# Optimization experiments

Hardware: AMD Instinct MI355X
Metric: run time of the kernel (lower is better)

## Reference

```python
import jax, jax.numpy as jnp
import numpy as np

B, S, H, E, V = 128, 400, 256, 128, 50000
PAD = 250  # extended-vocab padding hard-coded in the torch module


def setup_inputs() -> dict:
    key = jax.random.key(0)
    ks = jax.random.split(key, 20)
    return {
        "input_token": jax.random.randint(ks[0], (B, 1), 0, V),
        "last_decoder_hidden": jax.random.normal(ks[1], (B, H), jnp.float32),
        "encoder_states": jax.random.normal(ks[2], (B, S, H), jnp.float32),
        "full_input_var": jax.random.randint(ks[3], (B, S), 0, V + PAD),
        "emb_table": jax.random.normal(ks[4], (V, E), jnp.float32) * 0.02,
        "gru_w_ih": jax.random.normal(ks[5], (3 * H, E), jnp.float32) * 0.05,
        "gru_w_hh": jax.random.normal(ks[6], (3 * H, H), jnp.float32) * 0.05,
        "gru_b_ih": jax.random.normal(ks[7], (3 * H,), jnp.float32) * 0.05,
        "gru_b_hh": jax.random.normal(ks[8], (3 * H,), jnp.float32) * 0.05,
        "w_h": jax.random.normal(ks[9], (H,), jnp.float32),
        "w_s": jax.random.normal(ks[10], (H,), jnp.float32),
        "att_bias": jax.random.normal(ks[11], (1,), jnp.float32),
        "attn_v": jax.random.normal(ks[12], (H,), jnp.float32),
        "gen_w": jax.random.normal(ks[13], (1, 2 * H + E), jnp.float32) * 0.05,
        "gen_b": jax.random.normal(ks[14], (1,), jnp.float32) * 0.05,
        "outh_w": jax.random.normal(ks[15], (E, 2 * H), jnp.float32) * 0.05,
        "outh_b": jax.random.normal(ks[16], (E,), jnp.float32) * 0.05,
        "outv_w": jax.random.normal(ks[17], (V, E), jnp.float32) * 0.05,
        "outv_b": jax.random.normal(ks[18], (V,), jnp.float32) * 0.05,
    }


def reference(input_token, last_decoder_hidden, encoder_states, full_input_var,
              emb_table, gru_w_ih, gru_w_hh, gru_b_ih, gru_b_hh,
              w_h, w_s, att_bias, attn_v, gen_w, gen_b,
              outh_w, outh_b, outv_w, outv_b):
    b, s, h = encoder_states.shape
    v = outv_w.shape[0]
    # Embedding lookup (dropout is identity in eval mode): [B, E]
    x = emb_table[input_token[:, 0]]
    # Single-step GRU cell (PyTorch gate order: r, z, n)
    gi = x @ gru_w_ih.T + gru_b_ih
    gh = last_decoder_hidden @ gru_w_hh.T + gru_b_hh
    i_r, i_z, i_n = jnp.split(gi, 3, axis=-1)
    h_r, h_z, h_n = jnp.split(gh, 3, axis=-1)
    r = jax.nn.sigmoid(i_r + h_r)
    z = jax.nn.sigmoid(i_z + h_z)
    n = jnp.tanh(i_n + r * h_n)
    h_new = (1.0 - z) * n + z * last_decoder_hidden  # [B, H]
    # Bahdanau-style elementwise attention
    att = jnp.tanh(w_h * encoder_states + w_s * h_new[:, None, :] + att_bias)  # [B,S,H]
    scores = jnp.einsum('bsh,h->bs', att, attn_v)
    att_dist = jax.nn.softmax(scores, axis=-1)  # [B, S]
    context = jnp.einsum('bs,bsh->bh', att_dist, encoder_states)  # [B, H]
    dec_ctx = jnp.concatenate([h_new, context], axis=-1)  # [B, 2H]
    p_vocab = jax.nn.softmax((dec_ctx @ outh_w.T + outh_b) @ outv_w.T + outv_b, axis=-1)  # [B, V]
    p_gen = jax.nn.sigmoid(jnp.concatenate([dec_ctx, x], axis=1) @ gen_w.T + gen_b)  # [B, 1]
    # Pointer scatter-add into extended vocab [B, V+PAD]
    rows = jnp.arange(b)[:, None]
    token_input_dist = jnp.zeros((b, v + PAD), p_vocab.dtype).at[rows, full_input_var].add(att_dist)
    p_final = jnp.concatenate([p_vocab * p_gen, jnp.zeros((b, PAD), p_vocab.dtype)], axis=1) \
              + (1.0 - p_gen) * token_input_dist
    return (h_new, p_final, p_gen, p_vocab, att_dist)
```

## Files before the change

### kernel.cpp

```cpp
#include <hip/hip_runtime.h>
#include <hip/hip_bf16.h>


#define B_ 128
#define S_ 400
#define H_ 256
#define E_ 128
#define V_ 50000
#define PAD_ 250
#define VP_ (V_ + PAD_)
#define NC_ 8
#define CS_ (S_ / NC_)
#define NSUM_ 16

typedef unsigned short ushort_t;
typedef __attribute__((ext_vector_type(8))) short bf16x8;
typedef __attribute__((ext_vector_type(4))) float f32x4;

__device__ __forceinline__ unsigned short f2bfu(float f) {
    __hip_bfloat16 h = __float2bfloat16(f);
    union { __hip_bfloat16 h; unsigned short u; } c;
    c.h = h;
    return c.u;
}

__device__ __forceinline__ float sigmoid_fast(float x) {
    return 1.0f / (1.0f + __expf(-x));
}

__device__ __forceinline__ float tanh_fast(float x) {
    return 1.0f - 2.0f / (__expf(2.0f * x) + 1.0f);
}

__device__ __forceinline__ float waveReduceSumAll(float v) {
#pragma unroll
    for (int off = 1; off < 64; off <<= 1) v += __shfl_xor(v, off, 64);
    return v;
}

__global__ __launch_bounds__(256) void k_gates(
    const int* __restrict__ token, const float* __restrict__ emb,
    const float* __restrict__ hprev,
    const float* __restrict__ w_ih, const float* __restrict__ w_hh,
    float* __restrict__ gi_ws, float* __restrict__ gh_ws) {
    __shared__ ushort_t xh[B_ * 264];
    __shared__ int toks[B_];
    int t = threadIdx.x;
    bool isIH = blockIdx.x < 12;
    if (isIH) {
        if (t < B_) toks[t] = token[t];
        __syncthreads();
#pragma unroll
        for (int i = 0; i < 16; i++) {
            int fidx = i * 256 + t;
            int b = fidx >> 5, k4 = fidx & 31;
            float4 q = *(const float4*)(emb + (size_t)toks[b] * E_ + k4 * 4);
            ushort4 u;
            u.x = f2bfu(q.x); u.y = f2bfu(q.y); u.z = f2bfu(q.z); u.w = f2bfu(q.w);
            *(ushort4*)&xh[b * 136 + k4 * 4] = u;
        }
    } else {
#pragma unroll
        for (int i = 0; i < 32; i++) {
            int fidx = i * 256 + t;
            int b = fidx >> 6, k4 = fidx & 63;
            float4 q = *(const float4*)(hprev + (size_t)b * H_ + k4 * 4);
            ushort4 u;
            u.x = f2bfu(q.x); u.y = f2bfu(q.y); u.z = f2bfu(q.z); u.w = f2bfu(q.w);
            *(ushort4*)&xh[b * 264 + k4 * 4] = u;
        }
    }
    __syncthreads();

    int wave = t >> 6, lane = t & 63, lm = lane & 15, quad = lane >> 4;
    int tile = (isIH ? blockIdx.x : blockIdx.x - 12) * 4 + wave;
    int v = tile * 16 + lm;
    int K = isIH ? E_ : H_;
    int pitch = isIH ? 136 : 264;
    const float* wrow = (isIH ? w_ih : w_hh) + (size_t)v * K;
    float* gout = isIH ? gi_ws : gh_ws;

    f32x4 acc[8];
#pragma unroll
    for (int bt = 0; bt < 8; bt++) acc[bt] = (f32x4){0.f, 0.f, 0.f, 0.f};

    for (int kc = 0; kc < (K >> 5); kc++) {
        int k0 = kc * 32 + quad * 8;
        float4 w0 = *(const float4*)(wrow + k0);
        float4 w1 = *(const float4*)(wrow + k0 + 4);
        bf16x8 bf;
        bf[0] = (short)f2bfu(w0.x); bf[1] = (short)f2bfu(w0.y);
        bf[2] = (short)f2bfu(w0.z); bf[3] = (short)f2bfu(w0.w);
        bf[4] = (short)f2bfu(w1.x); bf[5] = (short)f2bfu(w1.y);
        bf[6] = (short)f2bfu(w1.z); bf[7] = (short)f2bfu(w1.w);
#pragma unroll
        for (int bt = 0; bt < 8; bt++) {
            bf16x8 af = *(const bf16x8*)&xh[(bt * 16 + lm) * pitch + k0];
            acc[bt] = __builtin_amdgcn_mfma_f32_16x16x32_bf16(af, bf, acc[bt], 0, 0, 0);
        }
    }
#pragma unroll
    for (int bt = 0; bt < 8; bt++)
#pragma unroll
        for (int r = 0; r < 4; r++) {
            int b = bt * 16 + quad * 4 + r;
            gout[(size_t)b * 768 + v] = acc[bt][r];
        }
}

__global__ __launch_bounds__(256) void k_attn(
    const float* __restrict__ gi_ws, const float* __restrict__ gh_ws,
    const float* __restrict__ b_ih, const float* __restrict__ b_hh,
    const float* __restrict__ hprev,
    const float* __restrict__ enc,
    const float* __restrict__ w_h, const float* __restrict__ w_s,
    const float* __restrict__ att_bias, const float* __restrict__ attn_v,
    float* __restrict__ out_hnew,
    float* __restrict__ sc_ws, float* __restrict__ ml_ws, float* __restrict__ ctxp_ws) {
    int c = blockIdx.x, b = blockIdx.y;
    int t = threadIdx.x;
    int wave = t >> 6, lane = t & 63;
    __shared__ float whs[H_], vs[H_], cs[H_], cmerge[H_];
    __shared__ float mred[4], lred[4];

    {
        float ir = gi_ws[(size_t)b * 768 + t] + b_ih[t];
        float iz = gi_ws[(size_t)b * 768 + 256 + t] + b_ih[256 + t];
        float in_ = gi_ws[(size_t)b * 768 + 512 + t] + b_ih[512 + t];
        float hr = gh_ws[(size_t)b * 768 + t] + b_hh[t];
        float hz = gh_ws[(size_t)b * 768 + 256 + t] + b_hh[256 + t];
        float hn = gh_ws[(size_t)b * 768 + 512 + t] + b_hh[512 + t];
        float hp = hprev[(size_t)b * H_ + t];
        float r = sigmoid_fast(ir + hr);
        float z = sigmoid_fast(iz + hz);
        float n = tanh_fast(in_ + r * hn);
        float h = (1.0f - z) * n + z * hp;
        if (c == 0) out_hnew[(size_t)b * H_ + t] = h;
        whs[t] = w_h[t];
        vs[t] = attn_v[t];
        cs[t] = w_s[t] * h + att_bias[0];
        cmerge[t] = 0.0f;
    }
    __syncthreads();

    int h0 = lane * 4;
    float m_w = -1e30f, l_w = 0.0f;
    float cx0 = 0.f, cx1 = 0.f, cx2 = 0.f, cx3 = 0.f;
    for (int si = wave; si < CS_; si += 4) {
        int s = c * CS_ + si;
        float4 u = *(const float4*)(enc + ((size_t)(b * S_ + s)) * H_ + h0);
        float p = vs[h0 + 0] * tanh_fast(whs[h0 + 0] * u.x + cs[h0 + 0])
                + vs[h0 + 1] * tanh_fast(whs[h0 + 1] * u.y + cs[h0 + 1])
                + vs[h0 + 2] * tanh_fast(whs[h0 + 2] * u.z + cs[h0 + 2])
                + vs[h0 + 3] * tanh_fast(whs[h0 + 3] * u.w + cs[h0 + 3]);
        p = waveReduceSumAll(p);
        if (lane == 0) sc_ws[b * S_ + s] = p;
        float mn = fmaxf(m_w, p);
        float scale = __expf(m_w - mn);
        float w = __expf(p - mn);
        cx0 = cx0 * scale + w * u.x;
        cx1 = cx1 * scale + w * u.y;
        cx2 = cx2 * scale + w * u.z;
        cx3 = cx3 * scale + w * u.w;
        l_w = l_w * scale + w;
        m_w = mn;
    }
    if (lane == 0) mred[wave] = m_w;
    __syncthreads();
    float m_c = fmaxf(fmaxf(mred[0], mred[1]), fmaxf(mred[2], mred[3]));
    float wf = __expf(m_w - m_c);
    if (lane == 0) lred[wave] = l_w * wf;
    atomicAdd(&cmerge[h0 + 0], cx0 * wf);
    atomicAdd(&cmerge[h0 + 1], cx1 * wf);
    atomicAdd(&cmerge[h0 + 2], cx2 * wf);
    atomicAdd(&cmerge[h0 + 3], cx3 * wf);
    __syncthreads();
    if (t == 0) {
        ml_ws[(b * NC_ + c) * 2 + 0] = m_c;
        ml_ws[(b * NC_ + c) * 2 + 1] = lred[0] + lred[1] + lred[2] + lred[3];
    }
    ctxp_ws[(size_t)(b * NC_ + c) * H_ + t] = cmerge[t];
}

__global__ __launch_bounds__(1024) void k_combine(
    const float* __restrict__ sc_ws, const float* __restrict__ ml_ws,
    const float* __restrict__ ctxp_ws,
    const float* __restrict__ out_hnew,
    const int* __restrict__ token, const float* __restrict__ emb,
    const float* __restrict__ outh_w, const float* __restrict__ outh_b,
    const float* __restrict__ gen_w, const float* __restrict__ gen_b,
    float* __restrict__ out_attd, float* __restrict__ out_pgen,
    float* __restrict__ attd_ws, float* __restrict__ hidden_ws,
    float* __restrict__ pgen_ws, float* __restrict__ row_sum16) {
    int b = blockIdx.x;
    int t = threadIdx.x;
    int wave = t >> 6, lane = t & 63;
    __shared__ float ml[NC_ * 2];
    __shared__ float dc[2 * H_ + E_];
    __shared__ float r2[16];

    if (b == 0) {
        for (int i = t; i < NSUM_ * B_; i += 1024) row_sum16[i] = 0.0f;
    }
    if (t < NC_ * 2) ml[t] = ml_ws[b * NC_ * 2 + t];
    __syncthreads();
    float M = -1e30f;
#pragma unroll
    for (int c = 0; c < NC_; c++) M = fmaxf(M, ml[2 * c]);
    float L = 0.0f;
#pragma unroll
    for (int c = 0; c < NC_; c++) L += ml[2 * c + 1] * __expf(ml[2 * c] - M);
    float invL = 1.0f / L;

    if (t < S_) {
        float a = __expf(sc_ws[b * S_ + t] - M) * invL;
        attd_ws[b * S_ + t] = a;
        out_attd[(size_t)b * S_ + t] = a;
    }
    if (t < H_) {
        float acc = 0.0f;
#pragma unroll
        for (int c = 0; c < NC_; c++)
            acc += __expf(ml[2 * c] - M) * ctxp_ws[(size_t)(b * NC_ + c) * H_ + t];
        dc[t] = out_hnew[(size_t)b * H_ + t];
        dc[H_ + t] = acc * invL;
    }
    if (t < E_) dc[2 * H_ + t] = emb[(size_t)token[b] * E_ + t];
    __syncthreads();

    {
        int r = t >> 3, sub = t & 7;
        const float* wrow = outh_w + (size_t)r * (2 * H_);
        float acc = 0.0f;
#pragma unroll
        for (int i = 0; i < 16; i++) {
            int k = i * 32 + sub * 4;
            float4 q = *(const float4*)(wrow + k);
            acc += dc[k] * q.x + dc[k + 1] * q.y + dc[k + 2] * q.z + dc[k + 3] * q.w;
        }
        acc += __shfl_down(acc, 4, 64);
        acc += __shfl_down(acc, 2, 64);
        acc += __shfl_down(acc, 1, 64);
        if (sub == 0) hidden_ws[(size_t)b * E_ + r] = acc + outh_b[r];
    }
    float pp = (t < 2 * H_ + E_) ? dc[t] * gen_w[t] : 0.0f;
    pp = waveReduceSumAll(pp);
    if (lane == 0) r2[wave] = pp;
    __syncthreads();
    if (t == 0) {
        float g = 0.0f;
#pragma unroll
        for (int wv = 0; wv < 16; wv++) g += r2[wv];
        g = sigmoid_fast(g + gen_b[0]);
        pgen_ws[b] = g;
        out_pgen[b] = g;
    }
}

#define VT_TOTAL (V_ / 16)
#define HID_PITCH 136
__global__ __launch_bounds__(256) void k_vocab_mfma(
    const float* __restrict__ outv_w, const float* __restrict__ outv_b,
    const float* __restrict__ hidden_ws,
    float* __restrict__ out_pvocab, float* __restrict__ row_sum16) {
    __shared__ ushort_t hid[B_ * HID_PITCH];
    __shared__ float rsum[B_];
    int t = threadIdx.x;

    const float4* h4 = (const float4*)hidden_ws;
#pragma unroll
    for (int i = 0; i < 16; i++) {
        int fidx = i * 256 + t;
        float4 q = h4[fidx];
        int row = fidx >> 5;
        int col = (fidx & 31) << 2;
        ushort4 u;
        u.x = f2bfu(q.x); u.y = f2bfu(q.y); u.z = f2bfu(q.z); u.w = f2bfu(q.w);
        *(ushort4*)&hid[row * HID_PITCH + col] = u;
    }
    if (t < B_) rsum[t] = 0.0f;
    __syncthreads();

    int wave = t >> 6, lane = t & 63, lm = lane & 15, quad = lane >> 4;
    int vt = blockIdx.x * 4 + wave;

    if (vt < VT_TOTAL) {
        int v = vt * 16 + lm;
        const float* wrow = outv_w + (size_t)v * E_;

        f32x4 acc[8];
#pragma unroll
        for (int bt = 0; bt < 8; bt++) acc[bt] = (f32x4){0.f, 0.f, 0.f, 0.f};

#pragma unroll
        for (int kc = 0; kc < 4; kc++) {
            int k0 = kc * 32 + quad * 8;
            float4 w0 = *(const float4*)(wrow + k0);
            float4 w1 = *(const float4*)(wrow + k0 + 4);
            bf16x8 bf;
            bf[0] = (short)f2bfu(w0.x); bf[1] = (short)f2bfu(w0.y);
            bf[2] = (short)f2bfu(w0.z); bf[3] = (short)f2bfu(w0.w);
            bf[4] = (short)f2bfu(w1.x); bf[5] = (short)f2bfu(w1.y);
            bf[6] = (short)f2bfu(w1.z); bf[7] = (short)f2bfu(w1.w);
#pragma unroll
            for (int bt = 0; bt < 8; bt++) {
                bf16x8 af = *(const bf16x8*)&hid[(bt * 16 + lm) * HID_PITCH + k0];
                acc[bt] = __builtin_amdgcn_mfma_f32_16x16x32_bf16(af, bf, acc[bt], 0, 0, 0);
            }
        }

        float bias = outv_b[v];
#pragma unroll
        for (int bt = 0; bt < 8; bt++) {
#pragma unroll
            for (int r = 0; r < 4; r++) {
                int b = bt * 16 + quad * 4 + r;
                float e = __expf(fminf(acc[bt][r] + bias, 60.0f));
                out_pvocab[(size_t)b * V_ + v] = e;
                float s = e;
                s += __shfl_xor(s, 1);
                s += __shfl_xor(s, 2);
                s += __shfl_xor(s, 4);
                s += __shfl_xor(s, 8);
                if (lm == 0) atomicAdd(&rsum[b], s);
            }
        }
    }
    __syncthreads();
    if (t < B_) atomicAdd(&row_sum16[(blockIdx.x & (NSUM_ - 1)) * B_ + t], rsum[t]);
}

__global__ __launch_bounds__(256) void k_final(
    const float* __restrict__ row_sum16, const float* __restrict__ pgen_ws,
    float* __restrict__ out_pfinal, float* __restrict__ out_pvocab) {
    int b = blockIdx.y;
    int jbase = blockIdx.x * 2048;
    int t = threadIdx.x;
    float rs = 0.0f;
#pragma unroll
    for (int i = 0; i < NSUM_; i++) rs += row_sum16[i * B_ + b];
    float inv = 1.0f / rs;
    float pg = pgen_ws[b];
#pragma unroll
    for (int i = 0; i < 8; i++) {
        int j = jbase + i * 256 + t;
        if (j < VP_) {
            if (j < V_) {
                float p = out_pvocab[(size_t)b * V_ + j] * inv;
                out_pvocab[(size_t)b * V_ + j] = p;
                out_pfinal[(size_t)b * VP_ + j] = p * pg;
            } else {
                out_pfinal[(size_t)b * VP_ + j] = 0.0f;
            }
        }
    }
}

__global__ __launch_bounds__(256) void k_scatter(
    const int* __restrict__ fiv, const float* __restrict__ attd_ws,
    const float* __restrict__ pgen_ws, float* __restrict__ out_pfinal) {
    int b = blockIdx.x;
    int t = threadIdx.x;
    float omg = 1.0f - pgen_ws[b];
    for (int s = t; s < S_; s += 256) {
        int idx = fiv[b * S_ + s];
        float val = omg * attd_ws[b * S_ + s];
        atomicAdd(&out_pfinal[(size_t)b * VP_ + idx], val);
    }
}

extern "C" void kernel_launch(void* const* d_in, const int* in_sizes, int n_in,
                              void* d_out, int out_size, void* d_ws, size_t ws_size,
                              hipStream_t stream) {
    const int* token = (const int*)d_in[0];
    const float* hprev = (const float*)d_in[1];
    const float* enc = (const float*)d_in[2];
    const int* fiv = (const int*)d_in[3];
    const float* emb = (const float*)d_in[4];
    const float* w_ih = (const float*)d_in[5];
    const float* w_hh = (const float*)d_in[6];
    const float* b_ih = (const float*)d_in[7];
    const float* b_hh = (const float*)d_in[8];
    const float* w_h = (const float*)d_in[9];
    const float* w_s = (const float*)d_in[10];
    const float* att_bias = (const float*)d_in[11];
    const float* attn_v = (const float*)d_in[12];
    const float* gen_w = (const float*)d_in[13];
    const float* gen_b = (const float*)d_in[14];
    const float* outh_w = (const float*)d_in[15];
    const float* outh_b = (const float*)d_in[16];
    const float* outv_w = (const float*)d_in[17];
    const float* outv_b = (const float*)d_in[18];

    float* out = (float*)d_out;
    float* out_hnew = out;
    float* out_pfinal = out + (size_t)B_ * H_;
    float* out_pgen = out_pfinal + (size_t)B_ * VP_;
    float* out_pvocab = out_pgen + B_;
    float* out_attd = out_pvocab + (size_t)B_ * V_;

    float* wsf = (float*)d_ws;
    float* gi_ws = wsf;
    float* gh_ws = wsf + 98304;
    float* attd_ws = wsf + 196608;
    float* hidden_ws = wsf + 247808;
    float* pgen_ws = wsf + 264192;
    float* row_sum16 = wsf + 264320;
    float* sc_ws = wsf + 266368;
    float* ml_ws = wsf + 317568;
    float* ctxp_ws = wsf + 319616;

    k_gates<<<24, 256, 0, stream>>>(token, emb, hprev, w_ih, w_hh, gi_ws, gh_ws);
    k_attn<<<dim3(NC_, B_), 256, 0, stream>>>(gi_ws, gh_ws, b_ih, b_hh, hprev,
                                              enc, w_h, w_s, att_bias, attn_v,
                                              out_hnew, sc_ws, ml_ws, ctxp_ws);
    k_combine<<<B_, 1024, 0, stream>>>(sc_ws, ml_ws, ctxp_ws, out_hnew, token, emb,
                                       outh_w, outh_b, gen_w, gen_b,
                                       out_attd, out_pgen,
                                       attd_ws, hidden_ws, pgen_ws, row_sum16);
    k_vocab_mfma<<<782, 256, 0, stream>>>(outv_w, outv_b, hidden_ws, out_pvocab, row_sum16);
    k_final<<<dim3(25, B_), 256, 0, stream>>>(row_sum16, pgen_ws, out_pfinal, out_pvocab);
    k_scatter<<<B_, 256, 0, stream>>>(fiv, attd_ws, pgen_ws, out_pfinal);
}
```

Measured before the change: 227.2 us.

## Fuse attention with combine and final normalization with pointer scatter

Merges the chunked attention kernel and the combine kernel into one per-batch 1024-thread block, so scores stay in shared memory and the partial max/sum/context workspaces and their cross-kernel merge go away. It also merges the vocab normalization kernel with the scatter kernel, using float4 loads, and reads p_gen and att_dist from the output buffers. This removes two launches and the workspace round-trips. In exchange the attention grid drops from 1024 blocks to 128 and the final pass from 3200 blocks to 128, so parallelism over the GPU shrinks.

```diff
diff --git a/kernel.cpp b/kernel.cpp
--- a/kernel.cpp
+++ b/kernel.cpp
@@ -9,8 +9,6 @@
 #define V_ 50000
 #define PAD_ 250
 #define VP_ (V_ + PAD_)
-#define NC_ 8
-#define CS_ (S_ / NC_)
 #define NSUM_ 16
 
 typedef unsigned short ushort_t;
@@ -108,22 +106,31 @@
         }
 }
 
-__global__ __launch_bounds__(256) void k_attn(
+__global__ __launch_bounds__(1024) void k_attn_combine(
     const float* __restrict__ gi_ws, const float* __restrict__ gh_ws,
     const float* __restrict__ b_ih, const float* __restrict__ b_hh,
     const float* __restrict__ hprev,
     const float* __restrict__ enc,
     const float* __restrict__ w_h, const float* __restrict__ w_s,
     const float* __restrict__ att_bias, const float* __restrict__ attn_v,
-    float* __restrict__ out_hnew,
-    float* __restrict__ sc_ws, float* __restrict__ ml_ws, float* __restrict__ ctxp_ws) {
-    int c = blockIdx.x, b = blockIdx.y;
+    const int* __restrict__ token, const float* __restrict__ emb,
+    const float* __restrict__ outh_w, const float* __restrict__ outh_b,
+    const float* __restrict__ gen_w, const float* __restrict__ gen_b,
+    float* __restrict__ out_hnew, float* __restrict__ out_attd,
+    float* __restrict__ out_pgen,
+    float* __restrict__ hidden_ws, float* __restrict__ row_sum16) {
+    int b = blockIdx.x;
     int t = threadIdx.x;
     int wave = t >> 6, lane = t & 63;
     __shared__ float whs[H_], vs[H_], cs[H_], cmerge[H_];
-    __shared__ float mred[4], lred[4];
-
-    {
+    __shared__ float scl[S_];
+    __shared__ float mred[16], lred[16], r2[16];
+    __shared__ float dc[2 * H_ + E_];
+
+    if (b == 0) {
+        for (int i = t; i < NSUM_ * B_; i += 1024) row_sum16[i] = 0.0f;
+    }
+    if (t < H_) {
         float ir = gi_ws[(size_t)b * 768 + t] + b_ih[t];
         float iz = gi_ws[(size_t)b * 768 + 256 + t] + b_ih[256 + t];
         float in_ = gi_ws[(size_t)b * 768 + 512 + t] + b_ih[512 + t];
@@ -135,26 +142,31 @@
         float z = sigmoid_fast(iz + hz);
         float n = tanh_fast(in_ + r * hn);
         float h = (1.0f - z) * n + z * hp;
-        if (c == 0) out_hnew[(size_t)b * H_ + t] = h;
+        out_hnew[(size_t)b * H_ + t] = h;
+        dc[t] = h;
         whs[t] = w_h[t];
         vs[t] = attn_v[t];
         cs[t] = w_s[t] * h + att_bias[0];
         cmerge[t] = 0.0f;
     }
+    if (t < E_) dc[2 * H_ + t] = emb[(size_t)token[b] * E_ + t];
     __syncthreads();
 
     int h0 = lane * 4;
+    float wh0 = whs[h0], wh1 = whs[h0 + 1], wh2 = whs[h0 + 2], wh3 = whs[h0 + 3];
+    float vv0 = vs[h0], vv1 = vs[h0 + 1], vv2 = vs[h0 + 2], vv3 = vs[h0 + 3];
+    float cc0 = cs[h0], cc1 = cs[h0 + 1], cc2 = cs[h0 + 2], cc3 = cs[h0 + 3];
+
     float m_w = -1e30f, l_w = 0.0f;
     float cx0 = 0.f, cx1 = 0.f, cx2 = 0.f, cx3 = 0.f;
-    for (int si = wave; si < CS_; si += 4) {
-        int s = c * CS_ + si;
+    for (int s = wave; s < S_; s += 16) {
         float4 u = *(const float4*)(enc + ((size_t)(b * S_ + s)) * H_ + h0);
-        float p = vs[h0 + 0] * tanh_fast(whs[h0 + 0] * u.x + cs[h0 + 0])
-                + vs[h0 + 1] * tanh_fast(whs[h0 + 1] * u.y + cs[h0 + 1])
-                + vs[h0 + 2] * tanh_fast(whs[h0 + 2] * u.z + cs[h0 + 2])
-                + vs[h0 + 3] * tanh_fast(whs[h0 + 3] * u.w + cs[h0 + 3]);
+        float p = vv0 * tanh_fast(wh0 * u.x + cc0)
+                + vv1 * tanh_fast(wh1 * u.y + cc1)
+                + vv2 * tanh_fast(wh2 * u.z + cc2)
+                + vv3 * tanh_fast(wh3 * u.w + cc3);
         p = waveReduceSumAll(p);
-        if (lane == 0) sc_ws[b * S_ + s] = p;
+        if (lane == 0) scl[s] = p;
         float mn = fmaxf(m_w, p);
         float scale = __expf(m_w - mn);
         float w = __expf(p - mn);
@@ -167,65 +179,25 @@
     }
     if (lane == 0) mred[wave] = m_w;
     __syncthreads();
-    float m_c = fmaxf(fmaxf(mred[0], mred[1]), fmaxf(mred[2], mred[3]));
-    float wf = __expf(m_w - m_c);
+    float M = -1e30f;
+#pragma unroll
+    for (int i = 0; i < 16; i++) M = fmaxf(M, mred[i]);
+    float wf = __expf(m_w - M);
     if (lane == 0) lred[wave] = l_w * wf;
     atomicAdd(&cmerge[h0 + 0], cx0 * wf);
     atomicAdd(&cmerge[h0 + 1], cx1 * wf);
     atomicAdd(&cmerge[h0 + 2], cx2 * wf);
     atomicAdd(&cmerge[h0 + 3], cx3 * wf);
     __syncthreads();
-    if (t == 0) {
-        ml_ws[(b * NC_ + c) * 2 + 0] = m_c;
-        ml_ws[(b * NC_ + c) * 2 + 1] = lred[0] + lred[1] + lred[2] + lred[3];
-    }
-    ctxp_ws[(size_t)(b * NC_ + c) * H_ + t] = cmerge[t];
-}
-
-__global__ __launch_bounds__(1024) void k_combine(
-    const float* __restrict__ sc_ws, const float* __restrict__ ml_ws,
-    const float* __restrict__ ctxp_ws,
-    const float* __restrict__ out_hnew,
-    const int* __restrict__ token, const float* __restrict__ emb,
-    const float* __restrict__ outh_w, const float* __restrict__ outh_b,
-    const float* __restrict__ gen_w, const float* __restrict__ gen_b,
-    float* __restrict__ out_attd, float* __restrict__ out_pgen,
-    float* __restrict__ attd_ws, float* __restrict__ hidden_ws,
-    float* __restrict__ pgen_ws, float* __restrict__ row_sum16) {
-    int b = blockIdx.x;
-    int t = threadIdx.x;
-    int wave = t >> 6, lane = t & 63;
-    __shared__ float ml[NC_ * 2];
-    __shared__ float dc[2 * H_ + E_];
-    __shared__ float r2[16];
-
-    if (b == 0) {
-        for (int i = t; i < NSUM_ * B_; i += 1024) row_sum16[i] = 0.0f;
-    }
-    if (t < NC_ * 2) ml[t] = ml_ws[b * NC_ * 2 + t];
-    __syncthreads();
-    float M = -1e30f;
-#pragma unroll
-    for (int c = 0; c < NC_; c++) M = fmaxf(M, ml[2 * c]);
     float L = 0.0f;
 #pragma unroll
-    for (int c = 0; c < NC_; c++) L += ml[2 * c + 1] * __expf(ml[2 * c] - M);
+    for (int i = 0; i < 16; i++) L += lred[i];
     float invL = 1.0f / L;
 
-    if (t < S_) {
-        float a = __expf(sc_ws[b * S_ + t] - M) * invL;
-        attd_ws[b * S_ + t] = a;
-        out_attd[(size_t)b * S_ + t] = a;
-    }
-    if (t < H_) {
-        float acc = 0.0f;
-#pragma unroll
-        for (int c = 0; c < NC_; c++)
-            acc += __expf(ml[2 * c] - M) * ctxp_ws[(size_t)(b * NC_ + c) * H_ + t];
-        dc[t] = out_hnew[(size_t)b * H_ + t];
-        dc[H_ + t] = acc * invL;
-    }
-    if (t < E_) dc[2 * H_ + t] = emb[(size_t)token[b] * E_ + t];
+    for (int s = t; s < S_; s += 1024) {
+        out_attd[(size_t)b * S_ + s] = __expf(scl[s] - M) * invL;
+    }
+    if (t < H_) dc[H_ + t] = cmerge[t] * invL;
     __syncthreads();
 
     {
@@ -251,9 +223,7 @@
         float g = 0.0f;
 #pragma unroll
         for (int wv = 0; wv < 16; wv++) g += r2[wv];
-        g = sigmoid_fast(g + gen_b[0]);
-        pgen_ws[b] = g;
-        out_pgen[b] = g;
+        out_pgen[b] = sigmoid_fast(g + gen_b[0]);
     }
 }
 
@@ -330,42 +300,35 @@
     if (t < B_) atomicAdd(&row_sum16[(blockIdx.x & (NSUM_ - 1)) * B_ + t], rsum[t]);
 }
 
-__global__ __launch_bounds__(256) void k_final(
-    const float* __restrict__ row_sum16, const float* __restrict__ pgen_ws,
+__global__ __launch_bounds__(1024) void k_final_scatter(
+    const float* __restrict__ row_sum16, const float* __restrict__ pgen,
+    const int* __restrict__ fiv, const float* __restrict__ attd,
     float* __restrict__ out_pfinal, float* __restrict__ out_pvocab) {
-    int b = blockIdx.y;
-    int jbase = blockIdx.x * 2048;
+    int b = blockIdx.x;
     int t = threadIdx.x;
     float rs = 0.0f;
 #pragma unroll
     for (int i = 0; i < NSUM_; i++) rs += row_sum16[i * B_ + b];
     float inv = 1.0f / rs;
-    float pg = pgen_ws[b];
-#pragma unroll
-    for (int i = 0; i < 8; i++) {
-        int j = jbase + i * 256 + t;
-        if (j < VP_) {
-            if (j < V_) {
-                float p = out_pvocab[(size_t)b * V_ + j] * inv;
-                out_pvocab[(size_t)b * V_ + j] = p;
-                out_pfinal[(size_t)b * VP_ + j] = p * pg;
-            } else {
-                out_pfinal[(size_t)b * VP_ + j] = 0.0f;
-            }
-        }
-    }
-}
-
-__global__ __launch_bounds__(256) void k_scatter(
-    const int* __restrict__ fiv, const float* __restrict__ attd_ws,
-    const float* __restrict__ pgen_ws, float* __restrict__ out_pfinal) {
-    int b = blockIdx.x;
-    int t = threadIdx.x;
-    float omg = 1.0f - pgen_ws[b];
-    for (int s = t; s < S_; s += 256) {
-        int idx = fiv[b * S_ + s];
-        float val = omg * attd_ws[b * S_ + s];
-        atomicAdd(&out_pfinal[(size_t)b * VP_ + idx], val);
+    float pg = pgen[b];
+    float omg = 1.0f - pg;
+    float* pvrow = out_pvocab + (size_t)b * V_;
+    float* pfrow = out_pfinal + (size_t)b * VP_;
+
+    for (int i4 = t; i4 < V_ / 4; i4 += 1024) {
+        float4 p = *(float4*)(pvrow + i4 * 4);
+        p.x *= inv; p.y *= inv; p.z *= inv; p.w *= inv;
+        *(float4*)(pvrow + i4 * 4) = p;
+        float2 a; a.x = p.x * pg; a.y = p.y * pg;
+        float2 c; c.x = p.z * pg; c.y = p.w * pg;
+        *(float2*)(pfrow + i4 * 4) = a;
+        *(float2*)(pfrow + i4 * 4 + 2) = c;
+    }
+    if (t < PAD_) pfrow[V_ + t] = 0.0f;
+    __syncthreads();
+    if (t < S_) {
+        int idx = fiv[b * S_ + t];
+        atomicAdd(&pfrow[idx], omg * attd[(size_t)b * S_ + t]);
     }
 }
 
@@ -402,23 +365,16 @@
     float* wsf = (float*)d_ws;
     float* gi_ws = wsf;
     float* gh_ws = wsf + 98304;
-    float* attd_ws = wsf + 196608;
-    float* hidden_ws = wsf + 247808;
-    float* pgen_ws = wsf + 264192;
-    float* row_sum16 = wsf + 264320;
-    float* sc_ws = wsf + 266368;
-    float* ml_ws = wsf + 317568;
-    float* ctxp_ws = wsf + 319616;
+    float* hidden_ws = wsf + 196608;
+    float* row_sum16 = wsf + 212992;
 
     k_gates<<<24, 256, 0, stream>>>(token, emb, hprev, w_ih, w_hh, gi_ws, gh_ws);
-    k_attn<<<dim3(NC_, B_), 256, 0, stream>>>(gi_ws, gh_ws, b_ih, b_hh, hprev,
-                                              enc, w_h, w_s, att_bias, attn_v,
-                                              out_hnew, sc_ws, ml_ws, ctxp_ws);
-    k_combine<<<B_, 1024, 0, stream>>>(sc_ws, ml_ws, ctxp_ws, out_hnew, token, emb,
-                                       outh_w, outh_b, gen_w, gen_b,
-                                       out_attd, out_pgen,
-                                       attd_ws, hidden_ws, pgen_ws, row_sum16);
+    k_attn_combine<<<B_, 1024, 0, stream>>>(gi_ws, gh_ws, b_ih, b_hh, hprev,
+                                            enc, w_h, w_s, att_bias, attn_v,
+                                            token, emb, outh_w, outh_b, gen_w, gen_b,
+                                            out_hnew, out_attd, out_pgen,
+                                            hidden_ws, row_sum16);
     k_vocab_mfma<<<782, 256, 0, stream>>>(outv_w, outv_b, hidden_ws, out_pvocab, row_sum16);
-    k_final<<<dim3(25, B_), 256, 0, stream>>>(row_sum16, pgen_ws, out_pfinal, out_pvocab);
-    k_scatter<<<B_, 256, 0, stream>>>(fiv, attd_ws, pgen_ws, out_pfinal);
-}
+    k_final_scatter<<<B_, 1024, 0, stream>>>(row_sum16, out_pgen, fiv, out_attd,
+                                             out_pfinal, out_pvocab);
+}
```

Result: slower. 233.2 us (+2.7%).

## Recompute vocab logits in second pass instead of storing and renormalizing

Applied to the files above, without the earlier changes.

The vocab GEMM now runs twice: a first pass that only accumulates per-row exp sums, and a second pass that recomputes the logits and writes normalized p_vocab and p_final directly. This removes the write-then-read-modify-write of the large unnormalized probability buffer and the separate finalization kernel, in exchange for reading outv_w again and redoing the MFMA work. It also stores the hidden projection as bf16, moves the row-sum zeroing earlier, writes the pad zeros in the scatter kernel, and hoists attention weights into registers.

```diff
diff --git a/kernel.cpp b/kernel.cpp
--- a/kernel.cpp
+++ b/kernel.cpp
@@ -42,11 +42,15 @@
     const int* __restrict__ token, const float* __restrict__ emb,
     const float* __restrict__ hprev,
     const float* __restrict__ w_ih, const float* __restrict__ w_hh,
-    float* __restrict__ gi_ws, float* __restrict__ gh_ws) {
+    float* __restrict__ gi_ws, float* __restrict__ gh_ws,
+    float* __restrict__ row_sum16) {
     __shared__ ushort_t xh[B_ * 264];
     __shared__ int toks[B_];
     int t = threadIdx.x;
     bool isIH = blockIdx.x < 12;
+    if (blockIdx.x == 0) {
+        for (int i = t; i < NSUM_ * B_; i += 256) row_sum16[i] = 0.0f;
+    }
     if (isIH) {
         if (t < B_) toks[t] = token[t];
         __syncthreads();
@@ -144,15 +148,19 @@
     __syncthreads();
 
     int h0 = lane * 4;
+    float wh0 = whs[h0], wh1 = whs[h0 + 1], wh2 = whs[h0 + 2], wh3 = whs[h0 + 3];
+    float vv0 = vs[h0], vv1 = vs[h0 + 1], vv2 = vs[h0 + 2], vv3 = vs[h0 + 3];
+    float cc0 = cs[h0], cc1 = cs[h0 + 1], cc2 = cs[h0 + 2], cc3 = cs[h0 + 3];
+
     float m_w = -1e30f, l_w = 0.0f;
     float cx0 = 0.f, cx1 = 0.f, cx2 = 0.f, cx3 = 0.f;
     for (int si = wave; si < CS_; si += 4) {
         int s = c * CS_ + si;
         float4 u = *(const float4*)(enc + ((size_t)(b * S_ + s)) * H_ + h0);
-        float p = vs[h0 + 0] * tanh_fast(whs[h0 + 0] * u.x + cs[h0 + 0])
-                + vs[h0 + 1] * tanh_fast(whs[h0 + 1] * u.y + cs[h0 + 1])
-                + vs[h0 + 2] * tanh_fast(whs[h0 + 2] * u.z + cs[h0 + 2])
-                + vs[h0 + 3] * tanh_fast(whs[h0 + 3] * u.w + cs[h0 + 3]);
+        float p = vv0 * tanh_fast(wh0 * u.x + cc0)
+                + vv1 * tanh_fast(wh1 * u.y + cc1)
+                + vv2 * tanh_fast(wh2 * u.z + cc2)
+                + vv3 * tanh_fast(wh3 * u.w + cc3);
         p = waveReduceSumAll(p);
         if (lane == 0) sc_ws[b * S_ + s] = p;
         float mn = fmaxf(m_w, p);
@@ -190,8 +198,7 @@
     const float* __restrict__ outh_w, const float* __restrict__ outh_b,
     const float* __restrict__ gen_w, const float* __restrict__ gen_b,
     float* __restrict__ out_attd, float* __restrict__ out_pgen,
-    float* __restrict__ attd_ws, float* __restrict__ hidden_ws,
-    float* __restrict__ pgen_ws, float* __restrict__ row_sum16) {
+    ushort_t* __restrict__ hidbf_ws) {
     int b = blockIdx.x;
     int t = threadIdx.x;
     int wave = t >> 6, lane = t & 63;
@@ -199,9 +206,6 @@
     __shared__ float dc[2 * H_ + E_];
     __shared__ float r2[16];
 
-    if (b == 0) {
-        for (int i = t; i < NSUM_ * B_; i += 1024) row_sum16[i] = 0.0f;
-    }
     if (t < NC_ * 2) ml[t] = ml_ws[b * NC_ * 2 + t];
     __syncthreads();
     float M = -1e30f;
@@ -213,9 +217,7 @@
     float invL = 1.0f / L;
 
     if (t < S_) {
-        float a = __expf(sc_ws[b * S_ + t] - M) * invL;
-        attd_ws[b * S_ + t] = a;
-        out_attd[(size_t)b * S_ + t] = a;
+        out_attd[(size_t)b * S_ + t] = __expf(sc_ws[b * S_ + t] - M) * invL;
     }
     if (t < H_) {
         float acc = 0.0f;
@@ -241,7 +243,7 @@
         acc += __shfl_down(acc, 4, 64);
         acc += __shfl_down(acc, 2, 64);
         acc += __shfl_down(acc, 1, 64);
-        if (sub == 0) hidden_ws[(size_t)b * E_ + r] = acc + outh_b[r];
+        if (sub == 0) hidbf_ws[(size_t)b * E_ + r] = f2bfu(acc + outh_b[r]);
     }
     float pp = (t < 2 * H_ + E_) ? dc[t] * gen_w[t] : 0.0f;
     pp = waveReduceSumAll(pp);
@@ -251,33 +253,55 @@
         float g = 0.0f;
 #pragma unroll
         for (int wv = 0; wv < 16; wv++) g += r2[wv];
-        g = sigmoid_fast(g + gen_b[0]);
-        pgen_ws[b] = g;
-        out_pgen[b] = g;
+        out_pgen[b] = sigmoid_fast(g + gen_b[0]);
     }
 }
 
 #define VT_TOTAL (V_ / 16)
 #define HID_PITCH 136
-__global__ __launch_bounds__(256) void k_vocab_mfma(
+
+__device__ __forceinline__ void stage_hid(const ushort_t* __restrict__ hidbf_ws,
+                                          ushort_t* __restrict__ hid, int t) {
+    const uint4* src = (const uint4*)hidbf_ws;
+#pragma unroll
+    for (int i = 0; i < 16; i++) {
+        int i4 = i * 256 + t;
+        uint4 q = src[i4];
+        int row = i4 >> 4;
+        int col4 = (i4 & 15) * 4;
+        *(uint4*)&hid[row * HID_PITCH + col4 * 2] = q;
+    }
+}
+
+__device__ __forceinline__ void vocab_gemm(const ushort_t* __restrict__ hid,
+                                           const float* __restrict__ wrow,
+                                           int lm, int quad, f32x4 acc[8]) {
+#pragma unroll
+    for (int kc = 0; kc < 4; kc++) {
+        int k0 = kc * 32 + quad * 8;
+        float4 w0 = *(const float4*)(wrow + k0);
+        float4 w1 = *(const float4*)(wrow + k0 + 4);
+        bf16x8 bf;
+        bf[0] = (short)f2bfu(w0.x); bf[1] = (short)f2bfu(w0.y);
+        bf[2] = (short)f2bfu(w0.z); bf[3] = (short)f2bfu(w0.w);
+        bf[4] = (short)f2bfu(w1.x); bf[5] = (short)f2bfu(w1.y);
+        bf[6] = (short)f2bfu(w1.z); bf[7] = (short)f2bfu(w1.w);
+#pragma unroll
+        for (int bt = 0; bt < 8; bt++) {
+            bf16x8 af = *(const bf16x8*)&hid[(bt * 16 + lm) * HID_PITCH + k0];
+            acc[bt] = __builtin_amdgcn_mfma_f32_16x16x32_bf16(af, bf, acc[bt], 0, 0, 0);
+        }
+    }
+}
+
+__global__ __launch_bounds__(256) void k_vocab_sum(
     const float* __restrict__ outv_w, const float* __restrict__ outv_b,
-    const float* __restrict__ hidden_ws,
-    float* __restrict__ out_pvocab, float* __restrict__ row_sum16) {
+    const ushort_t* __restrict__ hidbf_ws,
+    float* __restrict__ row_sum16) {
     __shared__ ushort_t hid[B_ * HID_PITCH];
     __shared__ float rsum[B_];
     int t = threadIdx.x;
-
-    const float4* h4 = (const float4*)hidden_ws;
-#pragma unroll
-    for (int i = 0; i < 16; i++) {
-        int fidx = i * 256 + t;
-        float4 q = h4[fidx];
-        int row = fidx >> 5;
-        int col = (fidx & 31) << 2;
-        ushort4 u;
-        u.x = f2bfu(q.x); u.y = f2bfu(q.y); u.z = f2bfu(q.z); u.w = f2bfu(q.w);
-        *(ushort4*)&hid[row * HID_PITCH + col] = u;
-    }
+    stage_hid(hidbf_ws, hid, t);
     if (t < B_) rsum[t] = 0.0f;
     __syncthreads();
 
@@ -287,27 +311,10 @@
     if (vt < VT_TOTAL) {
         int v = vt * 16 + lm;
         const float* wrow = outv_w + (size_t)v * E_;
-
         f32x4 acc[8];
 #pragma unroll
         for (int bt = 0; bt < 8; bt++) acc[bt] = (f32x4){0.f, 0.f, 0.f, 0.f};
-
-#pragma unroll
-        for (int kc = 0; kc < 4; kc++) {
-            int k0 = kc * 32 + quad * 8;
-            float4 w0 = *(const float4*)(wrow + k0);
-            float4 w1 = *(const float4*)(wrow + k0 + 4);
-            bf16x8 bf;
-            bf[0] = (short)f2bfu(w0.x); bf[1] = (short)f2bfu(w0.y);
-            bf[2] = (short)f2bfu(w0.z); bf[3] = (short)f2bfu(w0.w);
-            bf[4] = (short)f2bfu(w1.x); bf[5] = (short)f2bfu(w1.y);
-            bf[6] = (short)f2bfu(w1.z); bf[7] = (short)f2bfu(w1.w);
-#pragma unroll
-            for (int bt = 0; bt < 8; bt++) {
-                bf16x8 af = *(const bf16x8*)&hid[(bt * 16 + lm) * HID_PITCH + k0];
-                acc[bt] = __builtin_amdgcn_mfma_f32_16x16x32_bf16(af, bf, acc[bt], 0, 0, 0);
-            }
-        }
+        vocab_gemm(hid, wrow, lm, quad, acc);
 
         float bias = outv_b[v];
 #pragma unroll
@@ -316,7 +323,6 @@
             for (int r = 0; r < 4; r++) {
                 int b = bt * 16 + quad * 4 + r;
                 float e = __expf(fminf(acc[bt][r] + bias, 60.0f));
-                out_pvocab[(size_t)b * V_ + v] = e;
                 float s = e;
                 s += __shfl_xor(s, 1);
                 s += __shfl_xor(s, 2);
@@ -330,42 +336,62 @@
     if (t < B_) atomicAdd(&row_sum16[(blockIdx.x & (NSUM_ - 1)) * B_ + t], rsum[t]);
 }
 
-__global__ __launch_bounds__(256) void k_final(
-    const float* __restrict__ row_sum16, const float* __restrict__ pgen_ws,
-    float* __restrict__ out_pfinal, float* __restrict__ out_pvocab) {
-    int b = blockIdx.y;
-    int jbase = blockIdx.x * 2048;
-    int t = threadIdx.x;
-    float rs = 0.0f;
-#pragma unroll
-    for (int i = 0; i < NSUM_; i++) rs += row_sum16[i * B_ + b];
-    float inv = 1.0f / rs;
-    float pg = pgen_ws[b];
-#pragma unroll
-    for (int i = 0; i < 8; i++) {
-        int j = jbase + i * 256 + t;
-        if (j < VP_) {
-            if (j < V_) {
-                float p = out_pvocab[(size_t)b * V_ + j] * inv;
-                out_pvocab[(size_t)b * V_ + j] = p;
-                out_pfinal[(size_t)b * VP_ + j] = p * pg;
-            } else {
-                out_pfinal[(size_t)b * VP_ + j] = 0.0f;
+__global__ __launch_bounds__(256) void k_vocab_write(
+    const float* __restrict__ outv_w, const float* __restrict__ outv_b,
+    const ushort_t* __restrict__ hidbf_ws,
+    const float* __restrict__ row_sum16, const float* __restrict__ pgen,
+    float* __restrict__ out_pvocab, float* __restrict__ out_pfinal) {
+    __shared__ ushort_t hid[B_ * HID_PITCH];
+    __shared__ float rsinv[B_], pgs[B_];
+    int t = threadIdx.x;
+    stage_hid(hidbf_ws, hid, t);
+    if (t < B_) {
+        float rs = 0.0f;
+#pragma unroll
+        for (int i = 0; i < NSUM_; i++) rs += row_sum16[i * B_ + t];
+        rsinv[t] = 1.0f / rs;
+        pgs[t] = pgen[t];
+    }
+    __syncthreads();
+
+    int wave = t >> 6, lane = t & 63, lm = lane & 15, quad = lane >> 4;
+    int vt = blockIdx.x * 4 + wave;
+
+    if (vt < VT_TOTAL) {
+        int v = vt * 16 + lm;
+        const float* wrow = outv_w + (size_t)v * E_;
+        f32x4 acc[8];
+#pragma unroll
+        for (int bt = 0; bt < 8; bt++) acc[bt] = (f32x4){0.f, 0.f, 0.f, 0.f};
+        vocab_gemm(hid, wrow, lm, quad, acc);
+
+        float bias = outv_b[v];
+#pragma unroll
+        for (int bt = 0; bt < 8; bt++) {
+#pragma unroll
+            for (int r = 0; r < 4; r++) {
+                int b = bt * 16 + quad * 4 + r;
+                float e = __expf(fminf(acc[bt][r] + bias, 60.0f));
+                float p = e * rsinv[b];
+                out_pvocab[(size_t)b * V_ + v] = p;
+                out_pfinal[(size_t)b * VP_ + v] = p * pgs[b];
             }
         }
     }
 }
 
 __global__ __launch_bounds__(256) void k_scatter(
-    const int* __restrict__ fiv, const float* __restrict__ attd_ws,
-    const float* __restrict__ pgen_ws, float* __restrict__ out_pfinal) {
+    const int* __restrict__ fiv, const float* __restrict__ attd,
+    const float* __restrict__ pgen, float* __restrict__ out_pfinal) {
     int b = blockIdx.x;
     int t = threadIdx.x;
-    float omg = 1.0f - pgen_ws[b];
+    float* pfrow = out_pfinal + (size_t)b * VP_;
+    if (t < PAD_) pfrow[V_ + t] = 0.0f;
+    __syncthreads();
+    float omg = 1.0f - pgen[b];
     for (int s = t; s < S_; s += 256) {
         int idx = fiv[b * S_ + s];
-        float val = omg * attd_ws[b * S_ + s];
-        atomicAdd(&out_pfinal[(size_t)b * VP_ + idx], val);
+        atomicAdd(&pfrow[idx], omg * attd[(size_t)b * S_ + s]);
     }
 }
 
@@ -402,23 +428,23 @@
     float* wsf = (float*)d_ws;
     float* gi_ws = wsf;
     float* gh_ws = wsf + 98304;
-    float* attd_ws = wsf + 196608;
-    float* hidden_ws = wsf + 247808;
-    float* pgen_ws = wsf + 264192;
-    float* row_sum16 = wsf + 264320;
-    float* sc_ws = wsf + 266368;
-    float* ml_ws = wsf + 317568;
-    float* ctxp_ws = wsf + 319616;
-
-    k_gates<<<24, 256, 0, stream>>>(token, emb, hprev, w_ih, w_hh, gi_ws, gh_ws);
+    float* row_sum16 = wsf + 196608;
+    float* sc_ws = wsf + 198656;
+    float* ml_ws = wsf + 249856;
+    float* ctxp_ws = wsf + 251904;
+    ushort_t* hidbf_ws = (ushort_t*)(wsf + 514048);
+
+    k_gates<<<24, 256, 0, stream>>>(token, emb, hprev, w_ih, w_hh,
+                                    gi_ws, gh_ws, row_sum16);
     k_attn<<<dim3(NC_, B_), 256, 0, stream>>>(gi_ws, gh_ws, b_ih, b_hh, hprev,
                                               enc, w_h, w_s, att_bias, attn_v,
                                               out_hnew, sc_ws, ml_ws, ctxp_ws);
     k_combine<<<B_, 1024, 0, stream>>>(sc_ws, ml_ws, ctxp_ws, out_hnew, token, emb,
                                        outh_w, outh_b, gen_w, gen_b,
-                                       out_attd, out_pgen,
-                                       attd_ws, hidden_ws, pgen_ws, row_sum16);
-    k_vocab_mfma<<<782, 256, 0, stream>>>(outv_w, outv_b, hidden_ws, out_pvocab, row_sum16);
-    k_final<<<dim3(25, B_), 256, 0, stream>>>(row_sum16, pgen_ws, out_pfinal, out_pvocab);
-    k_scatter<<<B_, 256, 0, stream>>>(fiv, attd_ws, pgen_ws, out_pfinal);
-}
+                                       out_attd, out_pgen, hidbf_ws);
+    k_vocab_sum<<<782, 256, 0, stream>>>(outv_w, outv_b, hidbf_ws, row_sum16);
+    k_vocab_write<<<782, 256, 0, stream>>>(outv_w, outv_b, hidbf_ws,
+                                           row_sum16, out_pgen,
+                                           out_pvocab, out_pfinal);
+    k_scatter<<<B_, 256, 0, stream>>>(fiv, out_attd, out_pgen, out_pfinal);
+}
```

Result: no change. 227.0 us (-0.1%).
